# Kernel tuning notes

Measured on AMD Instinct MI355X. Metric: run time of the kernel, lower is better.

Reference implementation:

```python
import jax, jax.numpy as jnp
import numpy as np

N_NODES = 100000
N_EDGES = 1600000
NUM_GRAPHS = 128


def _gcn_layer(x, W, b, senders, receivers, n_node):
    # Linear transform first (cheaper: feature dim small)
    x = x @ W + b  # [N, out]
    ones = jnp.ones(senders.shape[0], dtype=x.dtype)
    deg_s = jax.ops.segment_sum(ones, senders, n_node)     # out-degree
    deg_r = jax.ops.segment_sum(ones, receivers, n_node)   # in-degree
    # symmetric normalization: D^-1/2 A D^-1/2
    x = x * jax.lax.rsqrt(jnp.maximum(deg_s, 1.0))[:, None]
    x = jax.ops.segment_sum(x[senders], receivers, n_node)  # gather-scatter aggregation
    x = x * jax.lax.rsqrt(jnp.maximum(deg_r, 1.0))[:, None]
    return x


def setup_inputs() -> dict:
    key = jax.random.key(0)
    ks = jax.random.split(key, 10)
    x = jax.random.normal(ks[0], (N_NODES, 9), dtype=jnp.float32)
    senders = jax.random.randint(ks[1], (N_EDGES,), 0, N_NODES)
    receivers = jax.random.randint(ks[2], (N_EDGES,), 0, N_NODES)
    batch = jnp.sort(jax.random.randint(ks[3], (N_NODES,), 0, NUM_GRAPHS))
    # learned params (Dense: W [in,out], b [out]) with LeCun-normal-ish scale
    def dense(k, din, dout):
        return jax.random.normal(k, (din, dout), dtype=jnp.float32) / np.sqrt(din)
    W1 = dense(ks[4], 9, 64)
    b1 = jnp.zeros((64,), jnp.float32)
    W2 = dense(ks[5], 64, 128)
    b2 = jnp.zeros((128,), jnp.float32)
    W3 = dense(ks[6], 128, 2)
    b3 = jnp.zeros((2,), jnp.float32)
    return {"x": x, "senders": senders, "receivers": receivers, "batch": batch,
            "num_graphs": NUM_GRAPHS, "W1": W1, "b1": b1, "W2": W2, "b2": b2,
            "W3": W3, "b3": b3}


def reference(x, senders, receivers, batch, num_graphs, W1, b1, W2, b2, W3, b3):
    n_node = x.shape[0]
    x = jax.nn.relu(_gcn_layer(x, W1, b1, senders, receivers, n_node))
    x = jax.nn.relu(_gcn_layer(x, W2, b2, senders, receivers, n_node))
    x = _gcn_layer(x, W3, b3, senders, receivers, n_node)
    # graph-level pooling
    return jax.ops.segment_sum(x, batch, num_graphs)
```

## Files before the change

kernel.cpp:

```cpp
#include <hip/hip_runtime.h>
#include <hip/hip_bf16.h>
#include <cstddef>

#define NBMAX 512
#define BCAP 5120
#define BKCHUNK 3200

typedef unsigned short bf16t;
typedef __attribute__((ext_vector_type(8))) short short8;
typedef __attribute__((ext_vector_type(4))) float f32x4;

static __device__ __forceinline__ float2 up2(unsigned u) {
    return make_float2(__uint_as_float(u << 16), __uint_as_float(u & 0xffff0000u));
}
static __device__ __forceinline__ bf16t f2bf(float f) {
    unsigned u = __float_as_uint(f);
    u += 0x7fffu + ((u >> 16) & 1u);
    return (bf16t)(u >> 16);
}
static __device__ __forceinline__ unsigned pk2(float a, float b) {
    return (unsigned)f2bf(a) | ((unsigned)f2bf(b) << 16);
}

__global__ void k_bucket(const int* __restrict__ S, const int* __restrict__ R,
                         unsigned* __restrict__ bufR, unsigned char* __restrict__ bufS,
                         int* __restrict__ gCntR, int* __restrict__ gCntS,
                         const float* __restrict__ W2, bf16t* __restrict__ W2f,
                         int nE, int nB) {
    __shared__ int histR[NBMAX], lstR[NBMAX], baseR[NBMAX];
    __shared__ int histS[NBMAX], lstS[NBMAX], baseS[NBMAX];
    __shared__ int sm[256];
    __shared__ unsigned sortedR[BKCHUNK];
    __shared__ unsigned short bOfR[BKCHUNK];
    __shared__ unsigned char sortedS[BKCHUNK];
    __shared__ unsigned short bOfS[BKCHUNK];
    int t = threadIdx.x;
    int nSort = gridDim.x - 4;
    if (blockIdx.x >= nSort) {
        int tt = (blockIdx.x - nSort) * blockDim.x + t;
        if (tt < 1024) {
            int nt = tt >> 7, kh = (tt >> 6) & 1, lane = tt & 63;
            int n = nt * 16 + (lane & 15);
            int k0 = kh * 32 + (lane >> 4) * 8;
            uint4 p;
            p.x = pk2(W2[(k0 + 0) * 128 + n], W2[(k0 + 1) * 128 + n]);
            p.y = pk2(W2[(k0 + 2) * 128 + n], W2[(k0 + 3) * 128 + n]);
            p.z = pk2(W2[(k0 + 4) * 128 + n], W2[(k0 + 5) * 128 + n]);
            p.w = pk2(W2[(k0 + 6) * 128 + n], W2[(k0 + 7) * 128 + n]);
            ((uint4*)W2f)[tt] = p;
        }
        return;
    }
    for (int i = t; i < NBMAX; i += 256) { histR[i] = 0; histS[i] = 0; }
    __syncthreads();
    int chunk = (nE + nSort - 1) / nSort;
    int e0 = blockIdx.x * chunk;
    int e1 = min(e0 + chunk, nE);
    for (int e = e0 + t; e < e1; e += 256) {
        atomicAdd(&histR[R[e] >> 8], 1);
        atomicAdd(&histS[S[e] >> 8], 1);
    }
    __syncthreads();
    {
        int c0 = histR[2 * t], c1 = histR[2 * t + 1];
        int ps = c0 + c1;
        sm[t] = ps;
        __syncthreads();
        for (int off = 1; off < 256; off <<= 1) {
            int y = (t >= off) ? sm[t - off] : 0;
            __syncthreads();
            sm[t] += y;
            __syncthreads();
        }
        int ex = sm[t] - ps;
        lstR[2 * t] = ex;
        lstR[2 * t + 1] = ex + c0;
    }
    __syncthreads();
    {
        int c0 = histS[2 * t], c1 = histS[2 * t + 1];
        int ps = c0 + c1;
        sm[t] = ps;
        __syncthreads();
        for (int off = 1; off < 256; off <<= 1) {
            int y = (t >= off) ? sm[t - off] : 0;
            __syncthreads();
            sm[t] += y;
            __syncthreads();
        }
        int ex = sm[t] - ps;
        lstS[2 * t] = ex;
        lstS[2 * t + 1] = ex + c0;
    }
    __syncthreads();
    for (int i = t; i < nB; i += 256) {
        int cR = histR[i];
        baseR[i] = cR ? atomicAdd(&gCntR[i], cR) : 0;
        int cS = histS[i];
        baseS[i] = cS ? atomicAdd(&gCntS[i], cS) : 0;
    }
    for (int i = t; i < NBMAX; i += 256) { histR[i] = 0; histS[i] = 0; }
    __syncthreads();
    for (int e = e0 + t; e < e1; e += 256) {
        int r = R[e], s = S[e];
        int br = r >> 8;
        int p = lstR[br] + atomicAdd(&histR[br], 1);
        sortedR[p] = ((unsigned)(r & 255) << 24) | (unsigned)s;
        bOfR[p] = (unsigned short)br;
        int bs = s >> 8;
        int p2 = lstS[bs] + atomicAdd(&histS[bs], 1);
        sortedS[p2] = (unsigned char)(s & 255);
        bOfS[p2] = (unsigned short)bs;
    }
    __syncthreads();
    int cnt = e1 - e0;
    for (int i = t; i < cnt; i += 256) {
        int b = bOfR[i];
        int slot = baseR[b] + (i - lstR[b]);
        if (slot < BCAP) bufR[(size_t)b * BCAP + slot] = sortedR[i];
        int b2 = bOfS[i];
        int slot2 = baseS[b2] + (i - lstS[b2]);
        if (slot2 < BCAP) bufS[(size_t)b2 * BCAP + slot2] = sortedS[i];
    }
}

__global__ void k_pass2(const unsigned* __restrict__ bufR, const unsigned char* __restrict__ bufS,
                        const int* __restrict__ gCntR, const int* __restrict__ gCntS,
                        const float* __restrict__ x,
                        int* __restrict__ csr, int* __restrict__ cur, int* __restrict__ degR,
                        float* __restrict__ inv_r, float* __restrict__ inv_s,
                        bf16t* __restrict__ xs, int nN, int nB) {
    __shared__ int hist[256], incl[256], curs[256], histS[256];
    __shared__ int sm[256];
    __shared__ int gex[NBMAX];
    int t = threadIdx.x;
    int b = blockIdx.x;
    {
        int c0 = (2 * t < nB) ? gCntR[2 * t] : 0;
        int c1 = (2 * t + 1 < nB) ? gCntR[2 * t + 1] : 0;
        int ps = c0 + c1;
        sm[t] = ps;
        __syncthreads();
        for (int off = 1; off < 256; off <<= 1) {
            int y = (t >= off) ? sm[t - off] : 0;
            __syncthreads();
            sm[t] += y;
            __syncthreads();
        }
        int ex = sm[t] - ps;
        gex[2 * t] = ex;
        gex[2 * t + 1] = ex + c0;
    }
    hist[t] = 0; curs[t] = 0; histS[t] = 0;
    __syncthreads();
    int gb = gex[b];
    int cnt = gCntR[b];
    const unsigned* buf = bufR + (size_t)b * BCAP;
    for (int i = t; i < cnt; i += 256) atomicAdd(&hist[buf[i] >> 24], 1);
    __syncthreads();
    int v = hist[t];
    sm[t] = v;
    __syncthreads();
    for (int off = 1; off < 256; off <<= 1) {
        int y = (t >= off) ? sm[t - off] : 0;
        __syncthreads();
        sm[t] += y;
        __syncthreads();
    }
    incl[t] = sm[t];
    __syncthreads();
    int n0 = b << 8;
    int n = n0 + t;
    if (n < nN) {
        degR[n] = v;
        cur[n] = gb + incl[t];
        inv_r[n] = rsqrtf(fmaxf((float)v, 1.f));
    }
    for (int i = t; i < cnt; i += 256) {
        unsigned p = buf[i];
        int rl = p >> 24;
        int s = p & 0xFFFFFF;
        int pos = gb + (incl[rl] - hist[rl]) + atomicAdd(&curs[rl], 1);
        csr[pos] = s;
    }
    int cntS = gCntS[b];
    const unsigned char* bufs = bufS + (size_t)b * BCAP;
    for (int i = t; i < cntS; i += 256) atomicAdd(&histS[bufs[i]], 1);
    __syncthreads();
    if (n < nN) {
        float is = rsqrtf(fmaxf((float)histS[t], 1.f));
        inv_s[n] = is;
        float w[9];
#pragma unroll
        for (int k = 0; k < 9; k++) w[k] = x[(size_t)n * 9 + k] * is;
        uint4 pa, pb;
        pa.x = pk2(w[0], w[1]); pa.y = pk2(w[2], w[3]);
        pa.z = pk2(w[4], w[5]); pa.w = pk2(w[6], w[7]);
        pb.x = pk2(w[8], is);   pb.y = 0; pb.z = 0; pb.w = 0;
        uint4* o = (uint4*)(xs + (size_t)n * 16);
        o[0] = pa;
        o[1] = pb;
    }
}

__global__ void k_h1f(const unsigned* __restrict__ xs32, const float* __restrict__ W1,
                      const float* __restrict__ b1,
                      const int* __restrict__ csr, const int* __restrict__ cur,
                      const int* __restrict__ degR, const float* __restrict__ inv_r,
                      const float* __restrict__ inv_s,
                      bf16t* __restrict__ h1s, float* __restrict__ warr, int nN) {
    __shared__ float Wl[9 * 64];
    __shared__ float bl[64];
    for (int i = threadIdx.x; i < 9 * 64; i += blockDim.x) Wl[i] = W1[i];
    if (threadIdx.x < 64) bl[threadIdx.x] = b1[threadIdx.x];
    __syncthreads();
    int lane = threadIdx.x & 63;
    int wave = threadIdx.x >> 6;
    int n = blockIdx.x * 16 + wave * 4 + (lane >> 4);
    int ql = lane & 15;
    int g = ql >> 2;
    int f2 = ql & 3;
    int nc = min(n, nN - 1);
    int deg = degR[nc];
    int st = cur[nc] - deg;
    float4 A0 = {0.f, 0.f, 0.f, 0.f}, A1 = A0, A2 = A0, A3 = A0;
    int i = 0;
    for (; i + 16 <= deg; i += 16) {
        int ea = csr[st + i + g];
        int eb = csr[st + i + 4 + g];
        int ec = csr[st + i + 8 + g];
        int ed = csr[st + i + 12 + g];
        uint2 u0 = *(const uint2*)(xs32 + (size_t)ea * 8 + f2 * 2);
        uint2 u1 = *(const uint2*)(xs32 + (size_t)eb * 8 + f2 * 2);
        uint2 u2 = *(const uint2*)(xs32 + (size_t)ec * 8 + f2 * 2);
        uint2 u3 = *(const uint2*)(xs32 + (size_t)ed * 8 + f2 * 2);
        float2 a = up2(u0.x), b = up2(u0.y);
        A0.x += a.x; A0.y += a.y; A0.z += b.x; A0.w += b.y;
        a = up2(u1.x); b = up2(u1.y);
        A1.x += a.x; A1.y += a.y; A1.z += b.x; A1.w += b.y;
        a = up2(u2.x); b = up2(u2.y);
        A2.x += a.x; A2.y += a.y; A2.z += b.x; A2.w += b.y;
        a = up2(u3.x); b = up2(u3.y);
        A3.x += a.x; A3.y += a.y; A3.z += b.x; A3.w += b.y;
    }
    for (; i + 4 <= deg; i += 4) {
        int ea = csr[st + i + g];
        uint2 u0 = *(const uint2*)(xs32 + (size_t)ea * 8 + f2 * 2);
        float2 a = up2(u0.x), b = up2(u0.y);
        A0.x += a.x; A0.y += a.y; A0.z += b.x; A0.w += b.y;
    }
    if (g < deg - i) {
        int ea = csr[st + i + g];
        uint2 u0 = *(const uint2*)(xs32 + (size_t)ea * 8 + f2 * 2);
        float2 a = up2(u0.x), b = up2(u0.y);
        A1.x += a.x; A1.y += a.y; A1.z += b.x; A1.w += b.y;
    }
    float4 vq = {(A0.x + A1.x) + (A2.x + A3.x), (A0.y + A1.y) + (A2.y + A3.y),
                 (A0.z + A1.z) + (A2.z + A3.z), (A0.w + A1.w) + (A2.w + A3.w)};
    vq.x += __shfl_xor(vq.x, 4); vq.y += __shfl_xor(vq.y, 4);
    vq.z += __shfl_xor(vq.z, 4); vq.w += __shfl_xor(vq.w, 4);
    vq.x += __shfl_xor(vq.x, 8); vq.y += __shfl_xor(vq.y, 8);
    vq.z += __shfl_xor(vq.z, 8); vq.w += __shfl_xor(vq.w, 8);
    int base = lane & 48;
    float xv[9];
    xv[0] = __shfl(vq.x, base + 0); xv[1] = __shfl(vq.y, base + 0);
    xv[2] = __shfl(vq.z, base + 0); xv[3] = __shfl(vq.w, base + 0);
    xv[4] = __shfl(vq.x, base + 1); xv[5] = __shfl(vq.y, base + 1);
    xv[6] = __shfl(vq.z, base + 1); xv[7] = __shfl(vq.w, base + 1);
    xv[8] = __shfl(vq.x, base + 2);
    float w = __shfl(vq.y, base + 2);
    float ir = inv_r[nc];
    float is = inv_s[nc];
    int c0 = ql * 4;
    float acc[4];
#pragma unroll
    for (int j = 0; j < 4; j++) acc[j] = w * bl[c0 + j];
#pragma unroll
    for (int k = 0; k < 9; k++) {
        float4 wv = *(const float4*)(Wl + k * 64 + c0);
        acc[0] += xv[k] * wv.x;
        acc[1] += xv[k] * wv.y;
        acc[2] += xv[k] * wv.z;
        acc[3] += xv[k] * wv.w;
    }
    if (n < nN) {
        float v0 = fmaxf(acc[0] * ir, 0.f) * is;
        float v1 = fmaxf(acc[1] * ir, 0.f) * is;
        float v2 = fmaxf(acc[2] * ir, 0.f) * is;
        float v3 = fmaxf(acc[3] * ir, 0.f) * is;
        uint2 pv;
        pv.x = pk2(v0, v1);
        pv.y = pk2(v2, v3);
        *(uint2*)(h1s + (size_t)n * 64 + c0) = pv;
        if (ql == 0) warr[n] = w;
    }
}

__global__ void k_l2f(const unsigned* __restrict__ h32, const bf16t* __restrict__ W2f,
                      const float* __restrict__ b2, const float* __restrict__ W3,
                      const float* __restrict__ inv_r, const float* __restrict__ inv_s,
                      const float* __restrict__ warr,
                      const int* __restrict__ csr, const int* __restrict__ cur,
                      const int* __restrict__ degR,
                      float* __restrict__ t, float* __restrict__ dout, int outSize, int nN) {
    __shared__ float b2l[128];
    __shared__ float W3l[256];
    __shared__ unsigned zl[64 * 36];
    for (int i = threadIdx.x; i < 128; i += blockDim.x) b2l[i] = b2[i];
    for (int i = threadIdx.x; i < 256; i += blockDim.x) W3l[i] = W3[i];
    if (blockIdx.x == 0 && threadIdx.x < outSize) dout[threadIdx.x] = 0.f;
    int lane = threadIdx.x & 63;
    int wave = threadIdx.x >> 6;
    int n0w = blockIdx.x * 64 + wave * 16;
    int q = lane >> 4;
    int ql = lane & 15;
    for (int j = 0; j < 16; j++) {
        int nc = min(n0w + j, nN - 1);
        int deg = degR[nc];
        int st = cur[nc] - deg;
        float4 A0 = {0.f, 0.f, 0.f, 0.f}, A1 = A0, A2 = A0, A3 = A0;
        int i = 0;
        for (; i + 16 <= deg; i += 16) {
            int ea = csr[st + i + q];
            int eb = csr[st + i + 4 + q];
            int ec = csr[st + i + 8 + q];
            int ed = csr[st + i + 12 + q];
            uint2 u0 = *(const uint2*)(h32 + (size_t)ea * 32 + ql * 2);
            uint2 u1 = *(const uint2*)(h32 + (size_t)eb * 32 + ql * 2);
            uint2 u2 = *(const uint2*)(h32 + (size_t)ec * 32 + ql * 2);
            uint2 u3 = *(const uint2*)(h32 + (size_t)ed * 32 + ql * 2);
            float2 a = up2(u0.x), b = up2(u0.y);
            A0.x += a.x; A0.y += a.y; A0.z += b.x; A0.w += b.y;
            a = up2(u1.x); b = up2(u1.y);
            A1.x += a.x; A1.y += a.y; A1.z += b.x; A1.w += b.y;
            a = up2(u2.x); b = up2(u2.y);
            A2.x += a.x; A2.y += a.y; A2.z += b.x; A2.w += b.y;
            a = up2(u3.x); b = up2(u3.y);
            A3.x += a.x; A3.y += a.y; A3.z += b.x; A3.w += b.y;
        }
        for (; i + 4 <= deg; i += 4) {
            int ea = csr[st + i + q];
            uint2 u0 = *(const uint2*)(h32 + (size_t)ea * 32 + ql * 2);
            float2 a = up2(u0.x), b = up2(u0.y);
            A0.x += a.x; A0.y += a.y; A0.z += b.x; A0.w += b.y;
        }
        if (q < deg - i) {
            int ea = csr[st + i + q];
            uint2 u0 = *(const uint2*)(h32 + (size_t)ea * 32 + ql * 2);
            float2 a = up2(u0.x), b = up2(u0.y);
            A1.x += a.x; A1.y += a.y; A1.z += b.x; A1.w += b.y;
        }
        float4 v = {(A0.x + A1.x) + (A2.x + A3.x), (A0.y + A1.y) + (A2.y + A3.y),
                    (A0.z + A1.z) + (A2.z + A3.z), (A0.w + A1.w) + (A2.w + A3.w)};
        v.x += __shfl_xor(v.x, 16); v.y += __shfl_xor(v.y, 16);
        v.z += __shfl_xor(v.z, 16); v.w += __shfl_xor(v.w, 16);
        v.x += __shfl_xor(v.x, 32); v.y += __shfl_xor(v.y, 32);
        v.z += __shfl_xor(v.z, 32); v.w += __shfl_xor(v.w, 32);
        if (q == 0) {
            uint2 pv;
            pv.x = pk2(v.x, v.y);
            pv.y = pk2(v.z, v.w);
            *(uint2*)(zl + (wave * 16 + j) * 36 + ql * 2) = pv;
        }
    }
    __syncthreads();
    int m = ql;
    int row = wave * 16 + m;
    short8 afr0 = *(const short8*)(zl + row * 36 + q * 4);
    short8 afr1 = *(const short8*)(zl + row * 36 + 16 + q * 4);
    float w4[4], ir4[4], is4[4];
#pragma unroll
    for (int reg = 0; reg < 4; reg++) {
        int nr = min(n0w + q * 4 + reg, nN - 1);
        w4[reg] = warr[nr];
        ir4[reg] = inv_r[nr];
        is4[reg] = inv_s[nr];
    }
    float p0[4] = {0.f, 0.f, 0.f, 0.f}, p1[4] = {0.f, 0.f, 0.f, 0.f};
#pragma unroll
    for (int nt = 0; nt < 8; nt++) {
        short8 b0 = *(const short8*)(W2f + ((size_t)(nt * 2 + 0) * 64 + lane) * 8);
        short8 b1 = *(const short8*)(W2f + ((size_t)(nt * 2 + 1) * 64 + lane) * 8);
        f32x4 acc = {0.f, 0.f, 0.f, 0.f};
        acc = __builtin_amdgcn_mfma_f32_16x16x32_bf16(afr0, b0, acc, 0, 0, 0);
        acc = __builtin_amdgcn_mfma_f32_16x16x32_bf16(afr1, b1, acc, 0, 0, 0);
        int col = nt * 16 + m;
        float bc = b2l[col];
        float w30 = W3l[col * 2 + 0];
        float w31 = W3l[col * 2 + 1];
#pragma unroll
        for (int reg = 0; reg < 4; reg++) {
            float h = fmaxf((acc[reg] + w4[reg] * bc) * ir4[reg], 0.f) * is4[reg];
            p0[reg] += h * w30;
            p1[reg] += h * w31;
        }
    }
#pragma unroll
    for (int mask = 1; mask < 16; mask <<= 1) {
#pragma unroll
        for (int reg = 0; reg < 4; reg++) {
            p0[reg] += __shfl_xor(p0[reg], mask);
            p1[reg] += __shfl_xor(p1[reg], mask);
        }
    }
    if (m == 0) {
#pragma unroll
        for (int reg = 0; reg < 4; reg++) {
            int nr = n0w + q * 4 + reg;
            if (nr < nN) *(float2*)(t + (size_t)nr * 2) = make_float2(p0[reg], p1[reg]);
        }
    }
}

__global__ void k_poolg(const float* __restrict__ t, const float* __restrict__ inv_r,
                        const float* __restrict__ warr, const float* __restrict__ b3,
                        const int* __restrict__ csr, const int* __restrict__ cur,
                        const int* __restrict__ degR, const int* __restrict__ batch,
                        float* out, int nN, int outSize) {
    __shared__ float sm[256];
    for (int i = threadIdx.x; i < 256; i += blockDim.x) sm[i] = 0.f;
    __syncthreads();
    float b30 = b3[0], b31 = b3[1];
    int n = blockIdx.x * blockDim.x + threadIdx.x;
    if (n < nN) {
        int deg = degR[n];
        int st = cur[n] - deg;
        float a0 = 0.f, a1 = 0.f, c0 = 0.f, c1 = 0.f;
        float d0 = 0.f, d1 = 0.f, e0 = 0.f, e1 = 0.f;
        int i = 0;
        for (; i + 4 <= deg; i += 4) {
            int sa = csr[st + i], sb = csr[st + i + 1];
            int sc = csr[st + i + 2], sd = csr[st + i + 3];
            float2 va = ((const float2*)t)[sa];
            float2 vb = ((const float2*)t)[sb];
            float2 vc = ((const float2*)t)[sc];
            float2 vd = ((const float2*)t)[sd];
            a0 += va.x; a1 += va.y;
            c0 += vb.x; c1 += vb.y;
            d0 += vc.x; d1 += vc.y;
            e0 += vd.x; e1 += vd.y;
        }
        for (; i < deg; i++) {
            float2 va = ((const float2*)t)[csr[st + i]];
            a0 += va.x; a1 += va.y;
        }
        float ir = inv_r[n];
        float wb = warr[n] * ir;
        int g = batch[n];
        atomicAdd(&sm[2 * g + 0], ((a0 + c0) + (d0 + e0)) * ir + wb * b30);
        atomicAdd(&sm[2 * g + 1], ((a1 + c1) + (d1 + e1)) * ir + wb * b31);
    }
    __syncthreads();
    for (int i = threadIdx.x; i < outSize; i += blockDim.x) atomicAdd(&out[i], sm[i]);
}

extern "C" void kernel_launch(void* const* d_in, const int* in_sizes, int n_in,
                              void* d_out, int out_size, void* d_ws, size_t ws_size,
                              hipStream_t stream) {
    const float* x     = (const float*)d_in[0];
    const int*   S     = (const int*)d_in[1];
    const int*   R     = (const int*)d_in[2];
    const int*   batch = (const int*)d_in[3];
    const float* W1 = (const float*)d_in[5];
    const float* b1 = (const float*)d_in[6];
    const float* W2 = (const float*)d_in[7];
    const float* b2 = (const float*)d_in[8];
    const float* W3 = (const float*)d_in[9];
    const float* b3 = (const float*)d_in[10];

    int nN = in_sizes[0] / 9;
    int nE = in_sizes[1];
    int nB = (nN + 255) / 256;

    char* ws = (char*)d_ws;
    int*   cur   = (int*)ws;
    int*   degR  = cur + nN;
    float* inv_s = (float*)(degR + nN);
    float* inv_r = inv_s + nN;
    float* warr  = inv_r + nN;
    int*   gCntR = (int*)(warr + nN);
    int*   gCntS = gCntR + NBMAX;
    int*   csr   = gCntS + NBMAX;
    bf16t* xs    = (bf16t*)(csr + nE);
    bf16t* W2f   = xs + (size_t)nN * 16;
    char*  regA  = (char*)(W2f + 8192);
    unsigned*      bufR = (unsigned*)regA;
    unsigned char* bufS = (unsigned char*)(bufR + (size_t)NBMAX * BCAP);
    bf16t* h1s = (bf16t*)regA;
    float* t   = (float*)(regA + (size_t)NBMAX * BCAP * 5);

    const int B = 256;

    hipMemsetAsync(gCntR, 0, 2 * NBMAX * 4, stream);
    k_bucket<<<516, B, 0, stream>>>(S, R, bufR, bufS, gCntR, gCntS, W2, W2f, nE, nB);
    k_pass2<<<nB, B, 0, stream>>>(bufR, bufS, gCntR, gCntS, x, csr, cur, degR,
                                  inv_r, inv_s, xs, nN, nB);

    k_h1f<<<(nN + 15) / 16, B, 0, stream>>>((const unsigned*)xs, W1, b1, csr, cur, degR,
                                            inv_r, inv_s, h1s, warr, nN);

    k_l2f<<<(nN + 63) / 64, B, 0, stream>>>((const unsigned*)h1s, W2f, b2, W3,
                                            inv_r, inv_s, warr, csr, cur, degR,
                                            t, (float*)d_out, out_size, nN);

    k_poolg<<<(nN + B - 1) / B, B, 0, stream>>>(t, inv_r, warr, b3, csr, cur, degR, batch,
                                                (float*)d_out, nN, out_size);
}
```

Before: 229.7 us.

## Split pass2 into sender and receiver kernels, fuse layer-1 aggregation into CSR build

The old pass2 kernel is split in two. One kernel computes out-degree normalisation and the bf16 prescaled node features. The other builds the CSR and, in the same pass, aggregates layer-1 neighbour features into shared memory with LDS float atomics, then applies the 9x64 linear transform per node. This removes the separate k_h1f kernel and its second CSR traversal, at the cost of heavy LDS atomic contention and one thread computing 64 outputs per node. The layer-2 kernel also drops its shared-memory staging of b2/W3 and a barrier in favour of per-lane register loads. Workspace is re-laid out so h1s no longer aliases the bucket buffers.

```diff
diff --git a/kernel.cpp b/kernel.cpp
--- a/kernel.cpp
+++ b/kernel.cpp
@@ -124,17 +124,50 @@
     }
 }
 
-__global__ void k_pass2(const unsigned* __restrict__ bufR, const unsigned char* __restrict__ bufS,
-                        const int* __restrict__ gCntR, const int* __restrict__ gCntS,
-                        const float* __restrict__ x,
-                        int* __restrict__ csr, int* __restrict__ cur, int* __restrict__ degR,
-                        float* __restrict__ inv_r, float* __restrict__ inv_s,
-                        bf16t* __restrict__ xs, int nN, int nB) {
-    __shared__ int hist[256], incl[256], curs[256], histS[256];
-    __shared__ int sm[256];
-    __shared__ int gex[NBMAX];
+__global__ void k_pass2s(const unsigned char* __restrict__ bufS, const int* __restrict__ gCntS,
+                         const float* __restrict__ x,
+                         float* __restrict__ inv_s, bf16t* __restrict__ xs, int nN) {
+    __shared__ int histS[256];
     int t = threadIdx.x;
     int b = blockIdx.x;
+    histS[t] = 0;
+    __syncthreads();
+    int cntS = gCntS[b];
+    const unsigned char* bufs = bufS + (size_t)b * BCAP;
+    for (int i = t; i < cntS; i += 256) atomicAdd(&histS[bufs[i]], 1);
+    __syncthreads();
+    int n = (b << 8) + t;
+    if (n < nN) {
+        float is = rsqrtf(fmaxf((float)histS[t], 1.f));
+        inv_s[n] = is;
+        float w[9];
+#pragma unroll
+        for (int k = 0; k < 9; k++) w[k] = x[(size_t)n * 9 + k] * is;
+        uint4 pa, pb;
+        pa.x = pk2(w[0], w[1]); pa.y = pk2(w[2], w[3]);
+        pa.z = pk2(w[4], w[5]); pa.w = pk2(w[6], w[7]);
+        pb.x = pk2(w[8], is);   pb.y = 0; pb.z = 0; pb.w = 0;
+        uint4* o = (uint4*)(xs + (size_t)n * 16);
+        o[0] = pa;
+        o[1] = pb;
+    }
+}
+
+__global__ void k_pass2r(const unsigned* __restrict__ bufR, const int* __restrict__ gCntR,
+                         const unsigned* __restrict__ xs32, const float* __restrict__ W1,
+                         const float* __restrict__ b1, const float* __restrict__ inv_s,
+                         int* __restrict__ csr, int* __restrict__ cur, int* __restrict__ degR,
+                         float* __restrict__ inv_r, bf16t* __restrict__ h1s,
+                         float* __restrict__ warr, int nN, int nB) {
+    __shared__ int hist[256], curs[256], incl[256], sm[256];
+    __shared__ int gex[NBMAX];
+    __shared__ float zl[256 * 11];
+    __shared__ float Wl[9 * 64];
+    __shared__ float bl[64];
+    int t = threadIdx.x;
+    int b = blockIdx.x;
+    for (int i = t; i < 576; i += 256) Wl[i] = W1[i];
+    if (t < 64) bl[t] = b1[t];
     {
         int c0 = (2 * t < nB) ? gCntR[2 * t] : 0;
         int c1 = (2 * t + 1 < nB) ? gCntR[2 * t + 1] : 0;
@@ -151,7 +184,8 @@
         gex[2 * t] = ex;
         gex[2 * t + 1] = ex + c0;
     }
-    hist[t] = 0; curs[t] = 0; histS[t] = 0;
+    hist[t] = 0; curs[t] = 0;
+    for (int i = t; i < 256 * 11; i += 256) zl[i] = 0.f;
     __syncthreads();
     int gb = gex[b];
     int cnt = gCntR[b];
@@ -169,12 +203,12 @@
     }
     incl[t] = sm[t];
     __syncthreads();
-    int n0 = b << 8;
-    int n = n0 + t;
+    int n = (b << 8) + t;
+    float ir = rsqrtf(fmaxf((float)v, 1.f));
     if (n < nN) {
         degR[n] = v;
         cur[n] = gb + incl[t];
-        inv_r[n] = rsqrtf(fmaxf((float)v, 1.f));
+        inv_r[n] = ir;
     }
     for (int i = t; i < cnt; i += 256) {
         unsigned p = buf[i];
@@ -182,117 +216,48 @@
         int s = p & 0xFFFFFF;
         int pos = gb + (incl[rl] - hist[rl]) + atomicAdd(&curs[rl], 1);
         csr[pos] = s;
-    }
-    int cntS = gCntS[b];
-    const unsigned char* bufs = bufS + (size_t)b * BCAP;
-    for (int i = t; i < cntS; i += 256) atomicAdd(&histS[bufs[i]], 1);
+        uint4 u = *(const uint4*)(xs32 + (size_t)s * 8);
+        unsigned u4 = xs32[(size_t)s * 8 + 4];
+        float* zr = zl + rl * 11;
+        float2 f0 = up2(u.x), f1 = up2(u.y), f2v = up2(u.z), f3 = up2(u.w), f4 = up2(u4);
+        atomicAdd(zr + 0, f0.x);  atomicAdd(zr + 1, f0.y);
+        atomicAdd(zr + 2, f1.x);  atomicAdd(zr + 3, f1.y);
+        atomicAdd(zr + 4, f2v.x); atomicAdd(zr + 5, f2v.y);
+        atomicAdd(zr + 6, f3.x);  atomicAdd(zr + 7, f3.y);
+        atomicAdd(zr + 8, f4.x);  atomicAdd(zr + 9, f4.y);
+    }
     __syncthreads();
     if (n < nN) {
-        float is = rsqrtf(fmaxf((float)histS[t], 1.f));
-        inv_s[n] = is;
-        float w[9];
-#pragma unroll
-        for (int k = 0; k < 9; k++) w[k] = x[(size_t)n * 9 + k] * is;
-        uint4 pa, pb;
-        pa.x = pk2(w[0], w[1]); pa.y = pk2(w[2], w[3]);
-        pa.z = pk2(w[4], w[5]); pa.w = pk2(w[6], w[7]);
-        pb.x = pk2(w[8], is);   pb.y = 0; pb.z = 0; pb.w = 0;
-        uint4* o = (uint4*)(xs + (size_t)n * 16);
-        o[0] = pa;
-        o[1] = pb;
-    }
-}
-
-__global__ void k_h1f(const unsigned* __restrict__ xs32, const float* __restrict__ W1,
-                      const float* __restrict__ b1,
-                      const int* __restrict__ csr, const int* __restrict__ cur,
-                      const int* __restrict__ degR, const float* __restrict__ inv_r,
-                      const float* __restrict__ inv_s,
-                      bf16t* __restrict__ h1s, float* __restrict__ warr, int nN) {
-    __shared__ float Wl[9 * 64];
-    __shared__ float bl[64];
-    for (int i = threadIdx.x; i < 9 * 64; i += blockDim.x) Wl[i] = W1[i];
-    if (threadIdx.x < 64) bl[threadIdx.x] = b1[threadIdx.x];
-    __syncthreads();
-    int lane = threadIdx.x & 63;
-    int wave = threadIdx.x >> 6;
-    int n = blockIdx.x * 16 + wave * 4 + (lane >> 4);
-    int ql = lane & 15;
-    int g = ql >> 2;
-    int f2 = ql & 3;
-    int nc = min(n, nN - 1);
-    int deg = degR[nc];
-    int st = cur[nc] - deg;
-    float4 A0 = {0.f, 0.f, 0.f, 0.f}, A1 = A0, A2 = A0, A3 = A0;
-    int i = 0;
-    for (; i + 16 <= deg; i += 16) {
-        int ea = csr[st + i + g];
-        int eb = csr[st + i + 4 + g];
-        int ec = csr[st + i + 8 + g];
-        int ed = csr[st + i + 12 + g];
-        uint2 u0 = *(const uint2*)(xs32 + (size_t)ea * 8 + f2 * 2);
-        uint2 u1 = *(const uint2*)(xs32 + (size_t)eb * 8 + f2 * 2);
-        uint2 u2 = *(const uint2*)(xs32 + (size_t)ec * 8 + f2 * 2);
-        uint2 u3 = *(const uint2*)(xs32 + (size_t)ed * 8 + f2 * 2);
-        float2 a = up2(u0.x), b = up2(u0.y);
-        A0.x += a.x; A0.y += a.y; A0.z += b.x; A0.w += b.y;
-        a = up2(u1.x); b = up2(u1.y);
-        A1.x += a.x; A1.y += a.y; A1.z += b.x; A1.w += b.y;
-        a = up2(u2.x); b = up2(u2.y);
-        A2.x += a.x; A2.y += a.y; A2.z += b.x; A2.w += b.y;
-        a = up2(u3.x); b = up2(u3.y);
-        A3.x += a.x; A3.y += a.y; A3.z += b.x; A3.w += b.y;
-    }
-    for (; i + 4 <= deg; i += 4) {
-        int ea = csr[st + i + g];
-        uint2 u0 = *(const uint2*)(xs32 + (size_t)ea * 8 + f2 * 2);
-        float2 a = up2(u0.x), b = up2(u0.y);
-        A0.x += a.x; A0.y += a.y; A0.z += b.x; A0.w += b.y;
-    }
-    if (g < deg - i) {
-        int ea = csr[st + i + g];
-        uint2 u0 = *(const uint2*)(xs32 + (size_t)ea * 8 + f2 * 2);
-        float2 a = up2(u0.x), b = up2(u0.y);
-        A1.x += a.x; A1.y += a.y; A1.z += b.x; A1.w += b.y;
-    }
-    float4 vq = {(A0.x + A1.x) + (A2.x + A3.x), (A0.y + A1.y) + (A2.y + A3.y),
-                 (A0.z + A1.z) + (A2.z + A3.z), (A0.w + A1.w) + (A2.w + A3.w)};
-    vq.x += __shfl_xor(vq.x, 4); vq.y += __shfl_xor(vq.y, 4);
-    vq.z += __shfl_xor(vq.z, 4); vq.w += __shfl_xor(vq.w, 4);
-    vq.x += __shfl_xor(vq.x, 8); vq.y += __shfl_xor(vq.y, 8);
-    vq.z += __shfl_xor(vq.z, 8); vq.w += __shfl_xor(vq.w, 8);
-    int base = lane & 48;
-    float xv[9];
-    xv[0] = __shfl(vq.x, base + 0); xv[1] = __shfl(vq.y, base + 0);
-    xv[2] = __shfl(vq.z, base + 0); xv[3] = __shfl(vq.w, base + 0);
-    xv[4] = __shfl(vq.x, base + 1); xv[5] = __shfl(vq.y, base + 1);
-    xv[6] = __shfl(vq.z, base + 1); xv[7] = __shfl(vq.w, base + 1);
-    xv[8] = __shfl(vq.x, base + 2);
-    float w = __shfl(vq.y, base + 2);
-    float ir = inv_r[nc];
-    float is = inv_s[nc];
-    int c0 = ql * 4;
-    float acc[4];
-#pragma unroll
-    for (int j = 0; j < 4; j++) acc[j] = w * bl[c0 + j];
-#pragma unroll
-    for (int k = 0; k < 9; k++) {
-        float4 wv = *(const float4*)(Wl + k * 64 + c0);
-        acc[0] += xv[k] * wv.x;
-        acc[1] += xv[k] * wv.y;
-        acc[2] += xv[k] * wv.z;
-        acc[3] += xv[k] * wv.w;
-    }
-    if (n < nN) {
-        float v0 = fmaxf(acc[0] * ir, 0.f) * is;
-        float v1 = fmaxf(acc[1] * ir, 0.f) * is;
-        float v2 = fmaxf(acc[2] * ir, 0.f) * is;
-        float v3 = fmaxf(acc[3] * ir, 0.f) * is;
-        uint2 pv;
-        pv.x = pk2(v0, v1);
-        pv.y = pk2(v2, v3);
-        *(uint2*)(h1s + (size_t)n * 64 + c0) = pv;
-        if (ql == 0) warr[n] = w;
+        float xv[9];
+#pragma unroll
+        for (int k = 0; k < 9; k++) xv[k] = zl[t * 11 + k];
+        float w = zl[t * 11 + 9];
+        warr[n] = w;
+        float is = inv_s[n];
+        bf16t* o = h1s + (size_t)n * 64;
+#pragma unroll
+        for (int c = 0; c < 4; c++) {
+            float acc[16];
+#pragma unroll
+            for (int j = 0; j < 16; j++) acc[j] = w * bl[c * 16 + j];
+#pragma unroll
+            for (int k = 0; k < 9; k++) {
+#pragma unroll
+                for (int j = 0; j < 16; j++) acc[j] += xv[k] * Wl[k * 64 + c * 16 + j];
+            }
+            uint4 pv;
+            pv.x = pk2(fmaxf(acc[0] * ir, 0.f) * is,  fmaxf(acc[1] * ir, 0.f) * is);
+            pv.y = pk2(fmaxf(acc[2] * ir, 0.f) * is,  fmaxf(acc[3] * ir, 0.f) * is);
+            pv.z = pk2(fmaxf(acc[4] * ir, 0.f) * is,  fmaxf(acc[5] * ir, 0.f) * is);
+            pv.w = pk2(fmaxf(acc[6] * ir, 0.f) * is,  fmaxf(acc[7] * ir, 0.f) * is);
+            uint4 pw;
+            pw.x = pk2(fmaxf(acc[8] * ir, 0.f) * is,  fmaxf(acc[9] * ir, 0.f) * is);
+            pw.y = pk2(fmaxf(acc[10] * ir, 0.f) * is, fmaxf(acc[11] * ir, 0.f) * is);
+            pw.z = pk2(fmaxf(acc[12] * ir, 0.f) * is, fmaxf(acc[13] * ir, 0.f) * is);
+            pw.w = pk2(fmaxf(acc[14] * ir, 0.f) * is, fmaxf(acc[15] * ir, 0.f) * is);
+            *(uint4*)(o + c * 16) = pv;
+            *(uint4*)(o + c * 16 + 8) = pw;
+        }
     }
 }
 
@@ -303,11 +268,7 @@
                       const int* __restrict__ csr, const int* __restrict__ cur,
                       const int* __restrict__ degR,
                       float* __restrict__ t, float* __restrict__ dout, int outSize, int nN) {
-    __shared__ float b2l[128];
-    __shared__ float W3l[256];
     __shared__ unsigned zl[64 * 36];
-    for (int i = threadIdx.x; i < 128; i += blockDim.x) b2l[i] = b2[i];
-    for (int i = threadIdx.x; i < 256; i += blockDim.x) W3l[i] = W3[i];
     if (blockIdx.x == 0 && threadIdx.x < outSize) dout[threadIdx.x] = 0.f;
     int lane = threadIdx.x & 63;
     int wave = threadIdx.x >> 6;
@@ -329,26 +290,26 @@
             uint2 u1 = *(const uint2*)(h32 + (size_t)eb * 32 + ql * 2);
             uint2 u2 = *(const uint2*)(h32 + (size_t)ec * 32 + ql * 2);
             uint2 u3 = *(const uint2*)(h32 + (size_t)ed * 32 + ql * 2);
-            float2 a = up2(u0.x), b = up2(u0.y);
-            A0.x += a.x; A0.y += a.y; A0.z += b.x; A0.w += b.y;
-            a = up2(u1.x); b = up2(u1.y);
-            A1.x += a.x; A1.y += a.y; A1.z += b.x; A1.w += b.y;
-            a = up2(u2.x); b = up2(u2.y);
-            A2.x += a.x; A2.y += a.y; A2.z += b.x; A2.w += b.y;
-            a = up2(u3.x); b = up2(u3.y);
-            A3.x += a.x; A3.y += a.y; A3.z += b.x; A3.w += b.y;
+            float2 a = up2(u0.x), bb = up2(u0.y);
+            A0.x += a.x; A0.y += a.y; A0.z += bb.x; A0.w += bb.y;
+            a = up2(u1.x); bb = up2(u1.y);
+            A1.x += a.x; A1.y += a.y; A1.z += bb.x; A1.w += bb.y;
+            a = up2(u2.x); bb = up2(u2.y);
+            A2.x += a.x; A2.y += a.y; A2.z += bb.x; A2.w += bb.y;
+            a = up2(u3.x); bb = up2(u3.y);
+            A3.x += a.x; A3.y += a.y; A3.z += bb.x; A3.w += bb.y;
         }
         for (; i + 4 <= deg; i += 4) {
             int ea = csr[st + i + q];
             uint2 u0 = *(const uint2*)(h32 + (size_t)ea * 32 + ql * 2);
-            float2 a = up2(u0.x), b = up2(u0.y);
-            A0.x += a.x; A0.y += a.y; A0.z += b.x; A0.w += b.y;
+            float2 a = up2(u0.x), bb = up2(u0.y);
+            A0.x += a.x; A0.y += a.y; A0.z += bb.x; A0.w += bb.y;
         }
         if (q < deg - i) {
             int ea = csr[st + i + q];
             uint2 u0 = *(const uint2*)(h32 + (size_t)ea * 32 + ql * 2);
-            float2 a = up2(u0.x), b = up2(u0.y);
-            A1.x += a.x; A1.y += a.y; A1.z += b.x; A1.w += b.y;
+            float2 a = up2(u0.x), bb = up2(u0.y);
+            A1.x += a.x; A1.y += a.y; A1.z += bb.x; A1.w += bb.y;
         }
         float4 v = {(A0.x + A1.x) + (A2.x + A3.x), (A0.y + A1.y) + (A2.y + A3.y),
                     (A0.z + A1.z) + (A2.z + A3.z), (A0.w + A1.w) + (A2.w + A3.w)};
@@ -363,8 +324,15 @@
             *(uint2*)(zl + (wave * 16 + j) * 36 + ql * 2) = pv;
         }
     }
-    __syncthreads();
     int m = ql;
+    float bc[8], w30[8], w31[8];
+#pragma unroll
+    for (int nt = 0; nt < 8; nt++) {
+        int col = nt * 16 + m;
+        bc[nt] = b2[col];
+        w30[nt] = W3[col * 2 + 0];
+        w31[nt] = W3[col * 2 + 1];
+    }
     int row = wave * 16 + m;
     short8 afr0 = *(const short8*)(zl + row * 36 + q * 4);
     short8 afr1 = *(const short8*)(zl + row * 36 + 16 + q * 4);
@@ -384,15 +352,11 @@
         f32x4 acc = {0.f, 0.f, 0.f, 0.f};
         acc = __builtin_amdgcn_mfma_f32_16x16x32_bf16(afr0, b0, acc, 0, 0, 0);
         acc = __builtin_amdgcn_mfma_f32_16x16x32_bf16(afr1, b1, acc, 0, 0, 0);
-        int col = nt * 16 + m;
-        float bc = b2l[col];
-        float w30 = W3l[col * 2 + 0];
-        float w31 = W3l[col * 2 + 1];
 #pragma unroll
         for (int reg = 0; reg < 4; reg++) {
-            float h = fmaxf((acc[reg] + w4[reg] * bc) * ir4[reg], 0.f) * is4[reg];
-            p0[reg] += h * w30;
-            p1[reg] += h * w31;
+            float h = fmaxf((acc[reg] + w4[reg] * bc[nt]) * ir4[reg], 0.f) * is4[reg];
+            p0[reg] += h * w30[nt];
+            p1[reg] += h * w31[nt];
         }
     }
 #pragma unroll
@@ -483,21 +447,18 @@
     int*   csr   = gCntS + NBMAX;
     bf16t* xs    = (bf16t*)(csr + nE);
     bf16t* W2f   = xs + (size_t)nN * 16;
-    char*  regA  = (char*)(W2f + 8192);
-    unsigned*      bufR = (unsigned*)regA;
+    unsigned*      bufR = (unsigned*)(W2f + 8192);
     unsigned char* bufS = (unsigned char*)(bufR + (size_t)NBMAX * BCAP);
-    bf16t* h1s = (bf16t*)regA;
-    float* t   = (float*)(regA + (size_t)NBMAX * BCAP * 5);
+    bf16t* h1s = (bf16t*)(bufS + (size_t)NBMAX * BCAP);
+    float* t   = (float*)(h1s + (size_t)nN * 64);
 
     const int B = 256;
 
     hipMemsetAsync(gCntR, 0, 2 * NBMAX * 4, stream);
     k_bucket<<<516, B, 0, stream>>>(S, R, bufR, bufS, gCntR, gCntS, W2, W2f, nE, nB);
-    k_pass2<<<nB, B, 0, stream>>>(bufR, bufS, gCntR, gCntS, x, csr, cur, degR,
-                                  inv_r, inv_s, xs, nN, nB);
-
-    k_h1f<<<(nN + 15) / 16, B, 0, stream>>>((const unsigned*)xs, W1, b1, csr, cur, degR,
-                                            inv_r, inv_s, h1s, warr, nN);
+    k_pass2s<<<nB, B, 0, stream>>>(bufS, gCntS, x, inv_s, xs, nN);
+    k_pass2r<<<nB, B, 0, stream>>>(bufR, gCntR, (const unsigned*)xs, W1, b1, inv_s,
+                                   csr, cur, degR, inv_r, h1s, warr, nN, nB);
 
     k_l2f<<<(nN + 63) / 64, B, 0, stream>>>((const unsigned*)h1s, W2f, b2, W3,
                                             inv_r, inv_s, warr, csr, cur, degR,
```

Measured after the change: 336.5 us. 1.46x slower.
